# Kernel tuning notes

Measured on AMD Instinct MI355X. Metric: run time of the kernel, lower is better.

Reference implementation:

```python
import jax, jax.numpy as jnp
import numpy as np
from jax import lax

DN = ('NCH', 'OIH', 'NCH')

def conv1d(x, w, b, pad=0):
    y = lax.conv_general_dilated(x, w, window_strides=(1,), padding=[(pad, pad)], dimension_numbers=DN)
    return y + b[None, :, None]

def conv_transpose1d(x, w_torch, b):
    # torch ConvTranspose1d weight: [C_in, C_out, K]; equivalent to full conv with flipped kernel
    k = w_torch.shape[-1]
    w = jnp.flip(jnp.transpose(w_torch, (1, 0, 2)), axis=-1)  # [C_out, C_in, K]
    y = lax.conv_general_dilated(x, w, window_strides=(1,), padding=[(k - 1, k - 1)], dimension_numbers=DN)
    return y + b[None, :, None]

def converter(signal, w1, b1, w2, b2, wt, bt, w3, b3):
    h = jax.nn.relu(conv1d(signal, w1, b1))          # [B,10,n-2]
    h = jax.nn.relu(conv1d(h, w2, b2))               # [B,10,n-2]
    h = jax.nn.relu(conv_transpose1d(h, wt, bt))     # [B,10,n]
    h = jax.nn.sigmoid(conv1d(h, w3, b3))            # [B,2,n]
    return h

def setup_inputs() -> dict:
    key = jax.random.key(0)
    ks = jax.random.split(key, 12)
    B, C, n = 32, 128, 8192
    signal = jax.random.normal(ks[0], (B, C, n), dtype=jnp.float32)
    curr_diag = jax.random.uniform(ks[1], (B, n - 1), dtype=jnp.float32) + 0.5
    s = 0.1
    return {
        'signal': signal,
        'curr_diag': curr_diag,
        'index_diag': 1,
        'w1': jax.random.normal(ks[2], (10, C, 3), dtype=jnp.float32) * s,
        'b1': jax.random.normal(ks[3], (10,), dtype=jnp.float32) * s,
        'w2': jax.random.normal(ks[4], (10, 10, 1), dtype=jnp.float32) * s,
        'b2': jax.random.normal(ks[5], (10,), dtype=jnp.float32) * s,
        'wt': jax.random.normal(ks[6], (10, 10, 3), dtype=jnp.float32) * s,
        'bt': jax.random.normal(ks[7], (10,), dtype=jnp.float32) * s,
        'w3': jax.random.normal(ks[8], (2, 10, 1), dtype=jnp.float32) * s,
        'b3': jax.random.normal(ks[9], (2,), dtype=jnp.float32) * s,
        'const': jnp.float32(0.99),
    }

def reference(signal, curr_diag, index_diag, w1, b1, w2, b2, wt, bt, w3, b3, const):
    n = signal.shape[-1]
    lr = converter(signal, w1, b1, w2, b2, wt, bt, w3, b3)  # [B,2,n]
    left, right = lr[:, 0, :], lr[:, 1, :]
    # diag_len = n - index_diag; next diag has length diag_len - 1
    mass_in = curr_diag[:, 1:] * right[:, 1:n - index_diag]
    mass_in = mass_in + curr_diag[:, :-1] * left[:, index_diag:n - 1]
    mass_out = right[:, 0:n - index_diag - 1] + left[:, index_diag + 1:n]
    next_diag = const * mass_in / mass_out
    next_diag = jnp.log(next_diag)
    next_diag = next_diag - jnp.mean(next_diag)
    return next_diag
```

## Files before the change

### kernel.cpp

```cpp
#include <hip/hip_runtime.h>
#include <math.h>

#define B      32
#define CIN    128
#define NN     8192
#define N1     8190
#define CH     10
#define TOUT   244
#define NTILE  34
#define SCOLS  256
#define CPC    16
#define NCHUNK (CIN / CPC)

__device__ __forceinline__ void load_lds16(const float* g, float* l)
{
    __builtin_amdgcn_global_load_lds(
        (const __attribute__((address_space(1))) void*)g,
        (__attribute__((address_space(3))) void*)l, 16, 0, 0);
}

__global__ void k0_prep(const float* __restrict__ w1, float* __restrict__ wT)
{
    const int i = blockIdx.x * 256 + threadIdx.x;
    if (i < CIN * 32) {
        const int ci = i >> 5, r = i & 31;
        float v = 0.f;
        if (r < 30) {
            const int o = r / 3, k = r - o * 3;
            v = w1[(o * CIN + ci) * 3 + k];
        }
        wT[i] = v;
    }
}

__global__ __launch_bounds__(256, 4) void k_main(
    const float* __restrict__ sig, const float* __restrict__ wT,
    const float* __restrict__ b1, const float* __restrict__ w2, const float* __restrict__ b2,
    const float* __restrict__ wt, const float* __restrict__ bt,
    const float* __restrict__ w3, const float* __restrict__ b3,
    const float* __restrict__ cd, const float* __restrict__ cstp,
    float* __restrict__ outv, float* __restrict__ bsums)
{
    __shared__ float sigb[CPC * SCOLS];
    __shared__ float h2s[CH * 256];
    __shared__ float lsh[256], rsh[256], red[256];

    const int tid  = threadIdx.x;
    const int lane = tid & 63;
    const int wv   = tid >> 6;
    const int b    = blockIdx.y;
    const int t0   = blockIdx.x * TOUT;

    int s0 = t0 - 4;
    if (s0 < 0) s0 = 0;
    if (s0 > NN - SCOLS) s0 = NN - SCOLS;
    const int d0 = t0 - s0;

    const float* gb = sig + (size_t)b * CIN * NN + s0 + lane * 4;

    const int tc = (tid < 254) ? tid : 253;

    float y[CH];
#pragma unroll
    for (int o = 0; o < CH; ++o) y[o] = b1[o];

    for (int c = 0; c < NCHUNK; ++c) {
        if (c) __syncthreads();
#pragma unroll
        for (int r = 0; r < 4; ++r) {
            const int ch = c * CPC + wv * 4 + r;
            load_lds16(gb + (size_t)ch * NN, &sigb[(wv * 4 + r) * SCOLS]);
        }
        __syncthreads();

        const float* wbase = wT + c * CPC * 32;
#pragma unroll
        for (int j = 0; j < CPC; ++j) {
            const float v0 = sigb[j * SCOLS + tc];
            const float v1 = sigb[j * SCOLS + tc + 1];
            const float v2 = sigb[j * SCOLS + tc + 2];
            const float* wrow = wbase + j * 32;
#pragma unroll
            for (int o = 0; o < CH; ++o) {
                y[o] = fmaf(wrow[o * 3 + 0], v0, y[o]);
                y[o] = fmaf(wrow[o * 3 + 1], v1, y[o]);
                y[o] = fmaf(wrow[o * 3 + 2], v2, y[o]);
            }
        }
    }

    const int g = s0 + tid;
#pragma unroll
    for (int o = 0; o < CH; ++o) y[o] = fmaxf(y[o], 0.f);
#pragma unroll
    for (int o = 0; o < CH; ++o) {
        float a = b2[o];
#pragma unroll
        for (int i = 0; i < CH; ++i) a = fmaf(w2[o * CH + i], y[i], a);
        h2s[o * 256 + tid] = (tid <= 253 && g < N1) ? fmaxf(a, 0.f) : 0.f;
    }
    __syncthreads();

    const int s = t0 + tid;
    if (tid <= TOUT + 2 && s < NN) {
        const int ib = tid + d0 - 2;
        float acc[CH];
#pragma unroll
        for (int o = 0; o < CH; ++o) acc[o] = bt[o];
#pragma unroll
        for (int i = 0; i < CH; ++i) {
            const float a0 = (ib >= 0)     ? h2s[i * 256 + ib]     : 0.f;
            const float a1 = (ib + 1 >= 0) ? h2s[i * 256 + ib + 1] : 0.f;
            const float a2 =                 h2s[i * 256 + ib + 2];
            const float* wp = wt + i * CH * 3;
#pragma unroll
            for (int o = 0; o < CH; ++o) {
                acc[o] = fmaf(wp[o * 3 + 0], a2, acc[o]);
                acc[o] = fmaf(wp[o * 3 + 1], a1, acc[o]);
                acc[o] = fmaf(wp[o * 3 + 2], a0, acc[o]);
            }
        }
        float l = b3[0], r = b3[1];
#pragma unroll
        for (int o = 0; o < CH; ++o) {
            const float h3 = fmaxf(acc[o], 0.f);
            l = fmaf(w3[o],      h3, l);
            r = fmaf(w3[CH + o], h3, r);
        }
        lsh[tid] = 1.f / (1.f + __expf(-l));
        rsh[tid] = 1.f / (1.f + __expf(-r));
    }
    __syncthreads();

    float vlog = 0.f;
    const int t = t0 + tid;
    if (tid < TOUT && t < N1) {
        const float c0 = cd[(size_t)b * (NN - 1) + t];
        const float c1 = cd[(size_t)b * (NN - 1) + t + 1];
        const float mi = c1 * rsh[tid + 1] + c0 * lsh[tid + 1];
        const float mo = rsh[tid] + lsh[tid + 2];
        vlog = __logf(cstp[0] * mi / mo);
        outv[(size_t)b * N1 + t] = vlog;
    }

    red[tid] = vlog;
    __syncthreads();
#pragma unroll
    for (int st = 128; st > 0; st >>= 1) {
        if (tid < st) red[tid] += red[tid + st];
        __syncthreads();
    }
    if (tid == 0) bsums[blockIdx.y * NTILE + blockIdx.x] = red[0];
}

__global__ __launch_bounds__(256) void k3_meansub(
    const float* __restrict__ bsums, float* __restrict__ outv, int n)
{
    __shared__ float red[256];
    const int tid = threadIdx.x;
    float s = 0.f;
    for (int i = tid; i < NTILE * B; i += 256) s += bsums[i];
    red[tid] = s;
    __syncthreads();
#pragma unroll
    for (int st = 128; st > 0; st >>= 1) {
        if (tid < st) red[tid] += red[tid + st];
        __syncthreads();
    }
    const float mean = red[0] / (float)(B * N1);
    __syncthreads();
    const int i = blockIdx.x * 256 + tid;
    if (i < n) outv[i] -= mean;
}

extern "C" void kernel_launch(void* const* d_in, const int* in_sizes, int n_in,
                              void* d_out, int out_size, void* d_ws, size_t ws_size,
                              hipStream_t stream)
{
    const float* sig = (const float*)d_in[0];
    const float* cd  = (const float*)d_in[1];
    const float* w1  = (const float*)d_in[3];
    const float* b1  = (const float*)d_in[4];
    const float* w2  = (const float*)d_in[5];
    const float* b2  = (const float*)d_in[6];
    const float* wt  = (const float*)d_in[7];
    const float* bt  = (const float*)d_in[8];
    const float* w3  = (const float*)d_in[9];
    const float* b3  = (const float*)d_in[10];
    const float* cst = (const float*)d_in[11];

    float* outv = (float*)d_out;

    float* ws   = (float*)d_ws;
    float* wT   = ws;
    float* bsum = wT + CIN * 32;

    dim3 blk(256);

    k0_prep   <<<dim3(16), blk, 0, stream>>>(w1, wT);
    k_main    <<<dim3(NTILE, B), blk, 0, stream>>>(sig, wT, b1, w2, b2,
                                                   wt, bt, w3, b3, cd, cst, outv, bsum);
    k3_meansub<<<dim3((out_size + 255) / 256), blk, 0, stream>>>(bsum, outv, out_size);
}
```

Before: 250.6 us.

## Double-buffer per-wave signal staging with async LDS loads and waitcnt

Replaces the block-wide 16-channel chunk load and barrier with per-wave, double-buffered 8-channel staging windows. Loads use 4-byte global_load_lds, and the next chunk is prefetched while the current one is consumed, synchronised with s_waitcnt vmcnt instead of __syncthreads. The output tile grows to 252 so fewer blocks (33 per batch) cover the row, and the last tile is clamped to overlap the previous one, with ownership masking so the mean is not double counted. Occupancy hint rises to 5 blocks per SIMD. The narrower 4-byte loads and the overlapping halo windows per wave add instruction count and redundant traffic.

```diff
diff --git a/kernel.cpp b/kernel.cpp
--- a/kernel.cpp
+++ b/kernel.cpp
@@ -6,17 +6,17 @@
 #define NN     8192
 #define N1     8190
 #define CH     10
-#define TOUT   244
-#define NTILE  34
-#define SCOLS  256
-#define CPC    16
-#define NCHUNK (CIN / CPC)
-
-__device__ __forceinline__ void load_lds16(const float* g, float* l)
+#define TOUT   252
+#define NTILE  33
+#define WR     72
+#define CPR    8
+#define NCHUNK (CIN / CPR)
+
+__device__ __forceinline__ void load_lds4(const float* g, float* l)
 {
     __builtin_amdgcn_global_load_lds(
         (const __attribute__((address_space(1))) void*)g,
-        (__attribute__((address_space(3))) void*)l, 16, 0, 0);
+        (__attribute__((address_space(3))) void*)l, 4, 0, 0);
 }
 
 __global__ void k0_prep(const float* __restrict__ w1, float* __restrict__ wT)
@@ -33,7 +33,7 @@
     }
 }
 
-__global__ __launch_bounds__(256, 4) void k_main(
+__global__ __launch_bounds__(256, 5) void k_main(
     const float* __restrict__ sig, const float* __restrict__ wT,
     const float* __restrict__ b1, const float* __restrict__ w2, const float* __restrict__ b2,
     const float* __restrict__ wt, const float* __restrict__ bt,
@@ -41,7 +41,7 @@
     const float* __restrict__ cd, const float* __restrict__ cstp,
     float* __restrict__ outv, float* __restrict__ bsums)
 {
-    __shared__ float sigb[CPC * SCOLS];
+    __shared__ float stg[4][2][CPR * WR];
     __shared__ float h2s[CH * 256];
     __shared__ float lsh[256], rsh[256], red[256];
 
@@ -49,37 +49,46 @@
     const int lane = tid & 63;
     const int wv   = tid >> 6;
     const int b    = blockIdx.y;
-    const int t0   = blockIdx.x * TOUT;
-
-    int s0 = t0 - 4;
-    if (s0 < 0) s0 = 0;
-    if (s0 > NN - SCOLS) s0 = NN - SCOLS;
-    const int d0 = t0 - s0;
-
-    const float* gb = sig + (size_t)b * CIN * NN + s0 + lane * 4;
-
-    const int tc = (tid < 254) ? tid : 253;
+
+    int t0 = blockIdx.x * TOUT;
+    if (t0 > N1 - TOUT) t0 = N1 - TOUT;
+
+    const int  g      = t0 - 2 + tid;
+    const bool gvalid = (g >= 0) && (g < N1);
+
+    const int gw0 = t0 - 2 + 64 * wv;
+    int lb = gw0;
+    if (lb < 0) lb = 0;
+    if (lb > NN - WR) lb = NN - WR;
+    const int dlt = gw0 - lb;
+    int ib = lane + dlt;
+    if (ib < 0) ib = 0;
+    if (ib > WR - 3) ib = WR - 3;
+
+    const float* grow = sig + (size_t)b * CIN * NN + lb + lane;
+    float* buf0 = &stg[wv][0][0];
+    float* buf1 = &stg[wv][1][0];
 
     float y[CH];
 #pragma unroll
     for (int o = 0; o < CH; ++o) y[o] = b1[o];
 
-    for (int c = 0; c < NCHUNK; ++c) {
-        if (c) __syncthreads();
-#pragma unroll
-        for (int r = 0; r < 4; ++r) {
-            const int ch = c * CPC + wv * 4 + r;
-            load_lds16(gb + (size_t)ch * NN, &sigb[(wv * 4 + r) * SCOLS]);
-        }
-        __syncthreads();
-
-        const float* wbase = wT + c * CPC * 32;
-#pragma unroll
-        for (int j = 0; j < CPC; ++j) {
-            const float v0 = sigb[j * SCOLS + tc];
-            const float v1 = sigb[j * SCOLS + tc + 1];
-            const float v2 = sigb[j * SCOLS + tc + 2];
-            const float* wrow = wbase + j * 32;
+    auto issue = [&](int c, float* bf) {
+#pragma unroll
+        for (int r = 0; r < CPR; ++r) {
+            const float* gp = grow + (size_t)(c * CPR + r) * NN;
+            load_lds4(gp,     bf + r * WR);
+            load_lds4(gp + 8, bf + r * WR + 8);
+        }
+    };
+    auto consume = [&](int c, const float* bf) {
+        const float* wbase = wT + c * CPR * 32;
+#pragma unroll
+        for (int r = 0; r < CPR; ++r) {
+            const float v0 = bf[r * WR + ib];
+            const float v1 = bf[r * WR + ib + 1];
+            const float v2 = bf[r * WR + ib + 2];
+            const float* wrow = wbase + r * 32;
 #pragma unroll
             for (int o = 0; o < CH; ++o) {
                 y[o] = fmaf(wrow[o * 3 + 0], v0, y[o]);
@@ -87,9 +96,21 @@
                 y[o] = fmaf(wrow[o * 3 + 2], v2, y[o]);
             }
         }
-    }
-
-    const int g = s0 + tid;
+    };
+
+    issue(0, buf0);
+    for (int c = 0; c < NCHUNK; ++c) {
+        float* cur = (c & 1) ? buf1 : buf0;
+        float* nxt = (c & 1) ? buf0 : buf1;
+        if (c + 1 < NCHUNK) {
+            issue(c + 1, nxt);
+            __builtin_amdgcn_s_waitcnt(0x4F70);
+        } else {
+            __builtin_amdgcn_s_waitcnt(0x0F70);
+        }
+        consume(c, cur);
+    }
+
 #pragma unroll
     for (int o = 0; o < CH; ++o) y[o] = fmaxf(y[o], 0.f);
 #pragma unroll
@@ -97,21 +118,19 @@
         float a = b2[o];
 #pragma unroll
         for (int i = 0; i < CH; ++i) a = fmaf(w2[o * CH + i], y[i], a);
-        h2s[o * 256 + tid] = (tid <= 253 && g < N1) ? fmaxf(a, 0.f) : 0.f;
-    }
-    __syncthreads();
-
-    const int s = t0 + tid;
-    if (tid <= TOUT + 2 && s < NN) {
-        const int ib = tid + d0 - 2;
+        h2s[o * 256 + tid] = gvalid ? fmaxf(a, 0.f) : 0.f;
+    }
+    __syncthreads();
+
+    if (tid <= 253) {
         float acc[CH];
 #pragma unroll
         for (int o = 0; o < CH; ++o) acc[o] = bt[o];
 #pragma unroll
         for (int i = 0; i < CH; ++i) {
-            const float a0 = (ib >= 0)     ? h2s[i * 256 + ib]     : 0.f;
-            const float a1 = (ib + 1 >= 0) ? h2s[i * 256 + ib + 1] : 0.f;
-            const float a2 =                 h2s[i * 256 + ib + 2];
+            const float a0 = h2s[i * 256 + tid];
+            const float a1 = h2s[i * 256 + tid + 1];
+            const float a2 = h2s[i * 256 + tid + 2];
             const float* wp = wt + i * CH * 3;
 #pragma unroll
             for (int o = 0; o < CH; ++o) {
@@ -133,17 +152,19 @@
     __syncthreads();
 
     float vlog = 0.f;
+    bool  owned = false;
     const int t = t0 + tid;
-    if (tid < TOUT && t < N1) {
+    if (tid < TOUT) {
         const float c0 = cd[(size_t)b * (NN - 1) + t];
         const float c1 = cd[(size_t)b * (NN - 1) + t + 1];
         const float mi = c1 * rsh[tid + 1] + c0 * lsh[tid + 1];
         const float mo = rsh[tid] + lsh[tid + 2];
         vlog = __logf(cstp[0] * mi / mo);
         outv[(size_t)b * N1 + t] = vlog;
-    }
-
-    red[tid] = vlog;
+        owned = (t >= blockIdx.x * TOUT);
+    }
+
+    red[tid] = owned ? vlog : 0.f;
     __syncthreads();
 #pragma unroll
     for (int st = 128; st > 0; st >>= 1) {
```

Result: no change. 250.5 us (-0.1%).
